# Kernel optimization log

Hardware: AMD Instinct MI355X
Metric: run time of the kernel (lower is better)

Reference implementation:

```python
import jax, jax.numpy as jnp
import numpy as np

N = 50000       # nodes
E = 800000      # edges
IN = 128        # in_channels
HID = 64        # hidden_channels
OUT = 32        # out_channels
H = 4           # heads
EH = 64         # edge_hidden_channels
EOUT = 2        # edge_out_channels
NEG_SLOPE = 0.2 # PyG GATConv default


def gat_conv(x, edge_index, W, att_src, att_dst, bias, num_nodes):
    """PyG GATConv, concat=False, add_self_loops=False, eval mode (no dropout).
    edge_attr is ignored because edge_dim=None (lin_edge is None in PyG).
    Returns (out [N, C], alpha [E, H])."""
    heads, C = att_src.shape
    xl = (x @ W).reshape(-1, heads, C)                 # [N, H, C]
    src, dst = edge_index[0], edge_index[1]
    a_src = jnp.sum(xl * att_src, axis=-1)             # [N, H]
    a_dst = jnp.sum(xl * att_dst, axis=-1)             # [N, H]
    alpha = jax.nn.leaky_relu(a_src[src] + a_dst[dst], NEG_SLOPE)  # [E, H]
    # segment softmax over destination nodes
    amax = jax.ops.segment_max(alpha, dst, num_segments=num_nodes)
    amax = jnp.where(jnp.isfinite(amax), amax, 0.0)
    ex = jnp.exp(alpha - amax[dst])
    denom = jax.ops.segment_sum(ex, dst, num_segments=num_nodes)
    alpha_n = ex / (denom[dst] + 1e-16)                # [E, H]
    msg = xl[src] * alpha_n[:, :, None]                # [E, H, C]
    out = jax.ops.segment_sum(msg, dst, num_segments=num_nodes)  # [N, H, C]
    out = out.mean(axis=1) + bias                      # concat=False -> head mean
    return out, alpha_n


def setup_inputs() -> dict:
    key = jax.random.key(0)
    ks = jax.random.split(key, 16)
    x = jax.random.normal(ks[0], (N, IN), dtype=jnp.float32)
    edge_index = jax.random.randint(ks[1], (2, E), 0, N, dtype=jnp.int32)
    edge_attr = jax.random.normal(ks[2], (E, 5), dtype=jnp.float32)
    s = lambda fan: 1.0 / np.sqrt(fan)
    W1 = jax.random.normal(ks[3], (IN, H * HID), dtype=jnp.float32) * s(IN)
    att1_src = jax.random.normal(ks[4], (H, HID), dtype=jnp.float32) * s(HID)
    att1_dst = jax.random.normal(ks[5], (H, HID), dtype=jnp.float32) * s(HID)
    b1 = jnp.zeros((HID,), dtype=jnp.float32)
    W3 = jax.random.normal(ks[6], (HID, H * OUT), dtype=jnp.float32) * s(HID)
    att3_src = jax.random.normal(ks[7], (H, OUT), dtype=jnp.float32) * s(OUT)
    att3_dst = jax.random.normal(ks[8], (H, OUT), dtype=jnp.float32) * s(OUT)
    b3 = jnp.zeros((OUT,), dtype=jnp.float32)
    EIN = 2 * OUT + H  # cat(out_src, alpha, out_dst)
    mW1 = jax.random.normal(ks[9], (EIN, EH), dtype=jnp.float32) * s(EIN)
    mb1 = jnp.zeros((EH,), dtype=jnp.float32)
    mW2 = jax.random.normal(ks[10], (EH, EOUT), dtype=jnp.float32) * s(EH)
    mb2 = jnp.zeros((EOUT,), dtype=jnp.float32)
    return {"x": x, "edge_index": edge_index, "edge_attr": edge_attr,
            "return_attention_weights": 1,
            "W1": W1, "att1_src": att1_src, "att1_dst": att1_dst, "b1": b1,
            "W3": W3, "att3_src": att3_src, "att3_dst": att3_dst, "b3": b3,
            "mW1": mW1, "mb1": mb1, "mW2": mW2, "mb2": mb2}


def reference(x, edge_index, edge_attr, return_attention_weights,
              W1, att1_src, att1_dst, b1, W3, att3_src, att3_dst, b3,
              mW1, mb1, mW2, mb2):
    edge_len = edge_attr.shape[0]  # == E (no self loops added)
    out, alpha = gat_conv(x, edge_index, W1, att1_src, att1_dst, b1, N)
    out, alpha = gat_conv(out, edge_index, W3, att3_src, att3_dst, b3, N)
    # F.dropout with training=False is the identity (eval mode)
    ei = edge_index[:, :edge_len]
    al = alpha[:edge_len, :]
    out_src = out[ei[0]]                                # [E, OUT]
    out_dst = out[ei[1]]                                # [E, OUT]
    edge_feat = jnp.concatenate([out_src, al, out_dst], axis=-1)  # [E, 2*OUT+H]
    h = jax.nn.relu(edge_feat @ mW1 + mb1)
    edge_out = h @ mW2 + mb2                            # [E, EOUT]
    return (out, edge_out)
```

## Files before the change

### kernel.cpp

```cpp
#include <hip/hip_runtime.h>
#include <hip/hip_fp16.h>

constexpr int NN   = 50000;
constexpr int EE   = 800000;
constexpr int INF  = 128;
constexpr int NH   = 4;
constexpr int GR64 = (NN + 63) / 64;
constexpr int EB   = (EE + 255) / 256;
constexpr int NCH  = (NN + 255) / 256;

struct __align__(8) h4 { __half2 a, b; };

__device__ __forceinline__ float elw(float a) {
    a = (a > 0.f) ? a : 0.2f * a;
    return __expf(a);
}


template <int CH, bool HOUT>
__device__ __forceinline__ void gemm_att_tile48(const float* __restrict__ A,
                                                const float* __restrict__ B,
                                                void* __restrict__ Cv,
                                                const float* __restrict__ att_s,
                                                const float* __restrict__ att_d,
                                                float* __restrict__ a_s,
                                                float* __restrict__ a_d,
                                                int N, int K, int M,
                                                int row0, int col0, int tid,
                                                float (*As)[68], float (*Bs)[132]) {
    const int tx = tid & 15, ty = tid >> 4;
    float acc[4][8] = {};

    for (int k0 = 0; k0 < K; k0 += 16) {
        {
            const int a_row = tid >> 2;
            const int a_k   = (tid & 3) * 4;
            const int gr    = row0 + a_row;
            float4 v = make_float4(0.f, 0.f, 0.f, 0.f);
            if (gr < N) v = *(const float4*)(A + (size_t)gr * K + k0 + a_k);
            As[a_k + 0][a_row] = v.x;
            As[a_k + 1][a_row] = v.y;
            As[a_k + 2][a_row] = v.z;
            As[a_k + 3][a_row] = v.w;
        }
        {
            const int b_k = tid >> 4;
            const int b_c = (tid & 15) * 8;
            const float* bp = B + (size_t)(k0 + b_k) * M + col0 + b_c;
            *(float4*)&Bs[b_k][b_c]     = *(const float4*)bp;
            *(float4*)&Bs[b_k][b_c + 4] = *(const float4*)(bp + 4);
        }
        __syncthreads();
        #pragma unroll
        for (int kk = 0; kk < 16; ++kk) {
            const float4 a  = *(const float4*)&As[kk][ty * 4];
            const float4 b0 = *(const float4*)&Bs[kk][tx * 4];
            const float4 b1 = *(const float4*)&Bs[kk][64 + tx * 4];
            const float av[4] = {a.x, a.y, a.z, a.w};
            const float bv[8] = {b0.x,b0.y,b0.z,b0.w,b1.x,b1.y,b1.z,b1.w};
            #pragma unroll
            for (int i = 0; i < 4; ++i)
                #pragma unroll
                for (int j = 0; j < 8; ++j)
                    acc[i][j] = fmaf(av[i], bv[j], acc[i][j]);
        }
        __syncthreads();
    }

    const int c0 = col0 + tx * 4;
    const int c1 = c0 + 64;
    const int head0 = c0 / CH, pos0 = c0 % CH;
    const int head1 = c1 / CH, pos1 = c1 % CH;
    float attS[8], attD[8];
    #pragma unroll
    for (int j = 0; j < 4; ++j) {
        attS[j]     = att_s[head0 * CH + pos0 + j];
        attD[j]     = att_d[head0 * CH + pos0 + j];
        attS[j + 4] = att_s[head1 * CH + pos1 + j];
        attD[j + 4] = att_d[head1 * CH + pos1 + j];
    }
    #pragma unroll
    for (int i = 0; i < 4; ++i) {
        const int r = row0 + ty * 4 + i;
        if (r < N) {
            if constexpr (HOUT) {
                __half* C = (__half*)Cv;
                __half* cp0 = C + (size_t)r * M + c0;
                __half* cp1 = C + (size_t)r * M + c1;
                *(__half2*)(cp0)     = __halves2half2(__float2half_rn(acc[i][0]), __float2half_rn(acc[i][1]));
                *(__half2*)(cp0 + 2) = __halves2half2(__float2half_rn(acc[i][2]), __float2half_rn(acc[i][3]));
                *(__half2*)(cp1)     = __halves2half2(__float2half_rn(acc[i][4]), __float2half_rn(acc[i][5]));
                *(__half2*)(cp1 + 2) = __halves2half2(__float2half_rn(acc[i][6]), __float2half_rn(acc[i][7]));
            } else {
                float* C = (float*)Cv;
                *(float4*)(C + (size_t)r * M + c0) = make_float4(acc[i][0], acc[i][1], acc[i][2], acc[i][3]);
                *(float4*)(C + (size_t)r * M + c1) = make_float4(acc[i][4], acc[i][5], acc[i][6], acc[i][7]);
            }
        }
        float ss0 = 0.f, sd0 = 0.f, ss1 = 0.f, sd1 = 0.f;
        #pragma unroll
        for (int j = 0; j < 4; ++j) {
            ss0 = fmaf(acc[i][j], attS[j], ss0);
            sd0 = fmaf(acc[i][j], attD[j], sd0);
            ss1 = fmaf(acc[i][j + 4], attS[j + 4], ss1);
            sd1 = fmaf(acc[i][j + 4], attD[j + 4], sd1);
        }
        #pragma unroll
        for (int msk = 1; msk < CH / 4; msk <<= 1) {
            ss0 += __shfl_xor(ss0, msk, 64);
            sd0 += __shfl_xor(sd0, msk, 64);
            ss1 += __shfl_xor(ss1, msk, 64);
            sd1 += __shfl_xor(sd1, msk, 64);
        }
        if ((tx & (CH / 4 - 1)) == 0 && r < N) {
            a_s[r * NH + head0] = ss0;
            a_d[r * NH + head0] = sd0;
            a_s[r * NH + head1] = ss1;
            a_d[r * NH + head1] = sd1;
        }
    }
}

__device__ __forceinline__ void gemm_pq_tile48(const float* __restrict__ A,
                                               const float* __restrict__ B,
                                               __half* __restrict__ C,
                                               int N, int K, int M,
                                               int row0, int col0, int tid,
                                               float (*As)[68], float (*Bs)[132]) {
    const int tx = tid & 15, ty = tid >> 4;
    float acc[4][8] = {};
    for (int k0 = 0; k0 < K; k0 += 16) {
        {
            const int a_row = tid >> 2;
            const int a_k   = (tid & 3) * 4;
            const int gr    = row0 + a_row;
            float4 v = make_float4(0.f, 0.f, 0.f, 0.f);
            if (gr < N) v = *(const float4*)(A + (size_t)gr * K + k0 + a_k);
            As[a_k + 0][a_row] = v.x;
            As[a_k + 1][a_row] = v.y;
            As[a_k + 2][a_row] = v.z;
            As[a_k + 3][a_row] = v.w;
        }
        {
            const int b_k = tid >> 4;
            const int b_c = (tid & 15) * 8;
            const float* bp = B + (size_t)(k0 + b_k) * M + col0 + b_c;
            *(float4*)&Bs[b_k][b_c]     = *(const float4*)bp;
            *(float4*)&Bs[b_k][b_c + 4] = *(const float4*)(bp + 4);
        }
        __syncthreads();
        #pragma unroll
        for (int kk = 0; kk < 16; ++kk) {
            const float4 a  = *(const float4*)&As[kk][ty * 4];
            const float4 b0 = *(const float4*)&Bs[kk][tx * 4];
            const float4 b1 = *(const float4*)&Bs[kk][64 + tx * 4];
            const float av[4] = {a.x, a.y, a.z, a.w};
            const float bv[8] = {b0.x,b0.y,b0.z,b0.w,b1.x,b1.y,b1.z,b1.w};
            #pragma unroll
            for (int i = 0; i < 4; ++i)
                #pragma unroll
                for (int j = 0; j < 8; ++j)
                    acc[i][j] = fmaf(av[i], bv[j], acc[i][j]);
        }
        __syncthreads();
    }
    const int c0 = col0 + tx * 4;
    const int c1 = c0 + 64;
    #pragma unroll
    for (int i = 0; i < 4; ++i) {
        const int r = row0 + ty * 4 + i;
        if (r < N) {
            __half* cp0 = C + (size_t)r * M + c0;
            __half* cp1 = C + (size_t)r * M + c1;
            *(__half2*)(cp0)     = __halves2half2(__float2half_rn(acc[i][0]), __float2half_rn(acc[i][1]));
            *(__half2*)(cp0 + 2) = __halves2half2(__float2half_rn(acc[i][2]), __float2half_rn(acc[i][3]));
            *(__half2*)(cp1)     = __halves2half2(__float2half_rn(acc[i][4]), __float2half_rn(acc[i][5]));
            *(__half2*)(cp1 + 2) = __halves2half2(__float2half_rn(acc[i][6]), __float2half_rn(acc[i][7]));
        }
    }
}


__device__ __forceinline__ void softagg1_node(int n, int lane,
                                              const int* __restrict__ rowptr,
                                              const int* __restrict__ psrc,
                                              const float* __restrict__ a_s,
                                              const float* __restrict__ a_d,
                                              const __half* __restrict__ xl,
                                              const float* __restrict__ bias,
                                              float* __restrict__ out) {
    const int r0 = rowptr[n], r1 = rowptr[n + 1];
    const int hh = lane >> 4;
    const float ad = a_d[n * NH + hh];

    const h4* X = (const h4*)xl;
    float4 A0 = {0,0,0,0}, A1 = {0,0,0,0}, A2 = {0,0,0,0}, A3 = {0,0,0,0};
    float sum = 0.f;
    int j = r0;
    for (; j + 7 < r1; j += 8) {
        const int s0 = psrc[j],     s1 = psrc[j + 1], s2 = psrc[j + 2], s3 = psrc[j + 3];
        const int s4 = psrc[j + 4], s5 = psrc[j + 5], s6 = psrc[j + 6], s7 = psrc[j + 7];
        const float w0 = elw(a_s[s0 * NH + hh] + ad);
        const float w1 = elw(a_s[s1 * NH + hh] + ad);
        const float w2 = elw(a_s[s2 * NH + hh] + ad);
        const float w3 = elw(a_s[s3 * NH + hh] + ad);
        const float w4 = elw(a_s[s4 * NH + hh] + ad);
        const float w5 = elw(a_s[s5 * NH + hh] + ad);
        const float w6 = elw(a_s[s6 * NH + hh] + ad);
        const float w7 = elw(a_s[s7 * NH + hh] + ad);
        sum += ((w0 + w1) + (w2 + w3)) + ((w4 + w5) + (w6 + w7));
        const h4 v0 = X[(size_t)s0 * 64 + lane];
        const h4 v1 = X[(size_t)s1 * 64 + lane];
        const h4 v2 = X[(size_t)s2 * 64 + lane];
        const h4 v3 = X[(size_t)s3 * 64 + lane];
        const h4 v4 = X[(size_t)s4 * 64 + lane];
        const h4 v5 = X[(size_t)s5 * 64 + lane];
        const h4 v6 = X[(size_t)s6 * 64 + lane];
        const h4 v7 = X[(size_t)s7 * 64 + lane];
        float2 l0 = __half22float2(v0.a), m0 = __half22float2(v0.b);
        float2 l1 = __half22float2(v1.a), m1 = __half22float2(v1.b);
        float2 l2 = __half22float2(v2.a), m2 = __half22float2(v2.b);
        float2 l3 = __half22float2(v3.a), m3 = __half22float2(v3.b);
        float2 l4 = __half22float2(v4.a), m4 = __half22float2(v4.b);
        float2 l5 = __half22float2(v5.a), m5 = __half22float2(v5.b);
        float2 l6 = __half22float2(v6.a), m6 = __half22float2(v6.b);
        float2 l7 = __half22float2(v7.a), m7 = __half22float2(v7.b);
        A0.x = fmaf(w0, l0.x, A0.x); A0.y = fmaf(w0, l0.y, A0.y);
        A0.z = fmaf(w0, m0.x, A0.z); A0.w = fmaf(w0, m0.y, A0.w);
        A1.x = fmaf(w1, l1.x, A1.x); A1.y = fmaf(w1, l1.y, A1.y);
        A1.z = fmaf(w1, m1.x, A1.z); A1.w = fmaf(w1, m1.y, A1.w);
        A2.x = fmaf(w2, l2.x, A2.x); A2.y = fmaf(w2, l2.y, A2.y);
        A2.z = fmaf(w2, m2.x, A2.z); A2.w = fmaf(w2, m2.y, A2.w);
        A3.x = fmaf(w3, l3.x, A3.x); A3.y = fmaf(w3, l3.y, A3.y);
        A3.z = fmaf(w3, m3.x, A3.z); A3.w = fmaf(w3, m3.y, A3.w);
        A0.x = fmaf(w4, l4.x, A0.x); A0.y = fmaf(w4, l4.y, A0.y);
        A0.z = fmaf(w4, m4.x, A0.z); A0.w = fmaf(w4, m4.y, A0.w);
        A1.x = fmaf(w5, l5.x, A1.x); A1.y = fmaf(w5, l5.y, A1.y);
        A1.z = fmaf(w5, m5.x, A1.z); A1.w = fmaf(w5, m5.y, A1.w);
        A2.x = fmaf(w6, l6.x, A2.x); A2.y = fmaf(w6, l6.y, A2.y);
        A2.z = fmaf(w6, m6.x, A2.z); A2.w = fmaf(w6, m6.y, A2.w);
        A3.x = fmaf(w7, l7.x, A3.x); A3.y = fmaf(w7, l7.y, A3.y);
        A3.z = fmaf(w7, m7.x, A3.z); A3.w = fmaf(w7, m7.y, A3.w);
    }
    for (; j < r1; ++j) {
        const int s0 = psrc[j];
        const float w0 = elw(a_s[s0 * NH + hh] + ad);
        sum += w0;
        const h4 v0 = X[(size_t)s0 * 64 + lane];
        float2 l0 = __half22float2(v0.a), m0 = __half22float2(v0.b);
        A0.x = fmaf(w0, l0.x, A0.x); A0.y = fmaf(w0, l0.y, A0.y);
        A0.z = fmaf(w0, m0.x, A0.z); A0.w = fmaf(w0, m0.y, A0.w);
    }
    const float inv = 1.f / (sum + 1e-30f);
    float4 t;
    t.x = ((A0.x + A1.x) + (A2.x + A3.x)) * inv;
    t.y = ((A0.y + A1.y) + (A2.y + A3.y)) * inv;
    t.z = ((A0.z + A1.z) + (A2.z + A3.z)) * inv;
    t.w = ((A0.w + A1.w) + (A2.w + A3.w)) * inv;
    #pragma unroll
    for (int msk = 16; msk < 64; msk <<= 1) {
        t.x += __shfl_xor(t.x, msk, 64);
        t.y += __shfl_xor(t.y, msk, 64);
        t.z += __shfl_xor(t.z, msk, 64);
        t.w += __shfl_xor(t.w, msk, 64);
    }
    if (lane < 16) {
        const float4 b = ((const float4*)bias)[lane];
        float4 o;
        o.x = t.x * 0.25f + b.x; o.y = t.y * 0.25f + b.y;
        o.z = t.z * 0.25f + b.z; o.w = t.w * 0.25f + b.w;
        ((float4*)out)[(size_t)n * 16 + lane] = o;
    }
}

__device__ __forceinline__ void softagg2_node(int n, int lane,
                                              const int* __restrict__ rowptr,
                                              const int* __restrict__ psrc,
                                              const float* __restrict__ a_s,
                                              const float* __restrict__ a_d,
                                              float* __restrict__ alpha_p,
                                              float* __restrict__ inv_s,
                                              const __half* __restrict__ xl,
                                              const float* __restrict__ bias,
                                              float* __restrict__ out) {
    const int r0 = rowptr[n], r1 = rowptr[n + 1];
    const int cl = lane & 31, half = lane >> 5, hh = cl >> 3;
    const float ad = a_d[n * NH + hh];
    const bool writer = (cl & 7) == 0;

    const h4* X = (const h4*)xl;
    float4 A0 = {0,0,0,0}, A1 = {0,0,0,0};
    float sum = 0.f;
    int j = r0;
    for (; j + 7 < r1; j += 8) {
        const int ja = j + half, jc = j + 2 + half, je = j + 4 + half, jg = j + 6 + half;
        const int sa = psrc[ja], sc = psrc[jc], se = psrc[je], sg = psrc[jg];
        const float wa = elw(a_s[sa * NH + hh] + ad);
        const float wc = elw(a_s[sc * NH + hh] + ad);
        const float we = elw(a_s[se * NH + hh] + ad);
        const float wg = elw(a_s[sg * NH + hh] + ad);
        if (writer) {
            alpha_p[ja * NH + hh] = wa; alpha_p[jc * NH + hh] = wc;
            alpha_p[je * NH + hh] = we; alpha_p[jg * NH + hh] = wg;
        }
        sum += (wa + wc) + (we + wg);
        const h4 va = X[(size_t)sa * 32 + cl];
        const h4 vc = X[(size_t)sc * 32 + cl];
        const h4 ve = X[(size_t)se * 32 + cl];
        const h4 vg = X[(size_t)sg * 32 + cl];
        const float2 la = __half22float2(va.a), ma = __half22float2(va.b);
        const float2 lc = __half22float2(vc.a), mc = __half22float2(vc.b);
        const float2 le = __half22float2(ve.a), me = __half22float2(ve.b);
        const float2 lg = __half22float2(vg.a), mg = __half22float2(vg.b);
        A0.x = fmaf(wa, la.x, A0.x); A0.y = fmaf(wa, la.y, A0.y);
        A0.z = fmaf(wa, ma.x, A0.z); A0.w = fmaf(wa, ma.y, A0.w);
        A1.x = fmaf(wc, lc.x, A1.x); A1.y = fmaf(wc, lc.y, A1.y);
        A1.z = fmaf(wc, mc.x, A1.z); A1.w = fmaf(wc, mc.y, A1.w);
        A0.x = fmaf(we, le.x, A0.x); A0.y = fmaf(we, le.y, A0.y);
        A0.z = fmaf(we, me.x, A0.z); A0.w = fmaf(we, me.y, A0.w);
        A1.x = fmaf(wg, lg.x, A1.x); A1.y = fmaf(wg, lg.y, A1.y);
        A1.z = fmaf(wg, mg.x, A1.z); A1.w = fmaf(wg, mg.y, A1.w);
    }
    for (; j < r1; j += 2) {
        const int ja = j + half;
        const bool valid = ja < r1;
        const int sa = psrc[valid ? ja : r0];
        float wa = 0.f;
        if (valid) {
            wa = elw(a_s[sa * NH + hh] + ad);
            if (writer) alpha_p[ja * NH + hh] = wa;
        }
        sum += wa;
        const h4 va = X[(size_t)sa * 32 + cl];
        const float2 la = __half22float2(va.a), ma = __half22float2(va.b);
        A0.x = fmaf(wa, la.x, A0.x); A0.y = fmaf(wa, la.y, A0.y);
        A0.z = fmaf(wa, ma.x, A0.z); A0.w = fmaf(wa, ma.y, A0.w);
    }
    sum += __shfl_xor(sum, 32, 64);
    const float inv = 1.f / (sum + 1e-30f);
    if (writer && half == 0) inv_s[n * NH + hh] = inv;

    float4 t;
    t.x = A0.x + A1.x; t.y = A0.y + A1.y; t.z = A0.z + A1.z; t.w = A0.w + A1.w;
    t.x += __shfl_xor(t.x, 32, 64);
    t.y += __shfl_xor(t.y, 32, 64);
    t.z += __shfl_xor(t.z, 32, 64);
    t.w += __shfl_xor(t.w, 32, 64);
    t.x *= inv; t.y *= inv; t.z *= inv; t.w *= inv;
    #pragma unroll
    for (int q = 0; q < 2; ++q) {
        const int msk = (q == 0) ? 8 : 16;
        t.x += __shfl_xor(t.x, msk, 64);
        t.y += __shfl_xor(t.y, msk, 64);
        t.z += __shfl_xor(t.z, msk, 64);
        t.w += __shfl_xor(t.w, msk, 64);
    }
    if (lane < 8) {
        const float4 b = ((const float4*)bias)[lane];
        float4 o;
        o.x = t.x * 0.25f + b.x; o.y = t.y * 0.25f + b.y;
        o.z = t.z * 0.25f + b.z; o.w = t.w * 0.25f + b.w;
        ((float4*)out)[(size_t)n * 8 + lane] = o;
    }
}


__global__ __launch_bounds__(256) void csr_gemm1_k(const int* __restrict__ ei,
                                                   int* __restrict__ deg,
                                                   const float* __restrict__ mW1,
                                                   float* __restrict__ W1pq,
                                                   const float* __restrict__ x,
                                                   const float* __restrict__ W1,
                                                   __half* __restrict__ xlh,
                                                   const float* __restrict__ att1s,
                                                   const float* __restrict__ att1d,
                                                   float* __restrict__ a_s,
                                                   float* __restrict__ a_d) {
    __shared__ float As[16][68];
    __shared__ float Bs[16][132];
    const int b = blockIdx.x;
    if (b < EB) {
        const int e = b * 256 + threadIdx.x;
        if (e < EE) atomicAdd(&deg[ei[EE + e]], 1);
    } else if (b < EB + 16) {
        const int idx = (b - EB) * 256 + threadIdx.x;
        if (idx < 32 * 128) {
            const int k = idx >> 7, jj = idx & 127;
            W1pq[idx] = (jj < 64) ? mW1[k * 64 + jj] : mW1[(36 + k) * 64 + (jj - 64)];
        }
    } else {
        const int t = b - EB - 16;
        gemm_att_tile48<64, true>(x, W1, xlh, att1s, att1d, a_s, a_d,
                                  NN, INF, NH * 64,
                                  (t % GR64) * 64, (t / GR64) * 128,
                                  threadIdx.x, As, Bs);
    }
}

template <int CH, bool HOUT>
__global__ __launch_bounds__(256) void gemm_att48_k(const float* __restrict__ A,
                                                    const float* __restrict__ B,
                                                    void* __restrict__ Cv,
                                                    const float* __restrict__ att_s,
                                                    const float* __restrict__ att_d,
                                                    float* __restrict__ a_s,
                                                    float* __restrict__ a_d,
                                                    int N, int K, int M) {
    __shared__ float As[16][68];
    __shared__ float Bs[16][132];
    gemm_att_tile48<CH, HOUT>(A, B, Cv, att_s, att_d, a_s, a_d, N, K, M,
                              blockIdx.x * 64, blockIdx.y * 128, threadIdx.x, As, Bs);
}

__global__ __launch_bounds__(256) void gemm_pq48_k(const float* __restrict__ A,
                                                   const float* __restrict__ B,
                                                   __half* __restrict__ C,
                                                   int N, int K, int M) {
    __shared__ float As[16][68];
    __shared__ float Bs[16][132];
    gemm_pq_tile48(A, B, C, N, K, M, blockIdx.x * 64, blockIdx.y * 128, threadIdx.x, As, Bs);
}

__global__ __launch_bounds__(256) void scan1_k(const int* __restrict__ deg,
                                               int* __restrict__ bsum) {
    __shared__ int sw[4];
    const int tid = threadIdx.x, lane = tid & 63, wv = tid >> 6;
    const int i = blockIdx.x * 256 + tid;
    int s = (i < NN) ? deg[i] : 0;
    #pragma unroll
    for (int d = 1; d < 64; d <<= 1) s += __shfl_xor(s, d, 64);
    if (lane == 0) sw[wv] = s;
    __syncthreads();
    if (tid == 0) bsum[blockIdx.x] = sw[0] + sw[1] + sw[2] + sw[3];
}

__global__ __launch_bounds__(256) void scan2_k(const int* __restrict__ bsum,
                                               int* __restrict__ boff) {
    __shared__ int sw[8];
    const int tid = threadIdx.x, lane = tid & 63, wv = tid >> 6;
    int v = (tid < NCH) ? bsum[tid] : 0;
    int incl = v;
    #pragma unroll
    for (int d = 1; d < 64; d <<= 1) {
        int t = __shfl_up(incl, d, 64);
        if (lane >= d) incl += t;
    }
    if (lane == 63) sw[wv] = incl;
    __syncthreads();
    if (wv == 0 && lane < 4) {
        int s4 = sw[lane];
        #pragma unroll
        for (int d = 1; d < 4; d <<= 1) {
            int t = __shfl_up(s4, d, 64);
            if (lane >= d) s4 += t;
        }
        sw[lane + 4] = s4;
    }
    __syncthreads();
    const int woff = (wv > 0) ? sw[wv - 1 + 4] : 0;
    if (tid < NCH) boff[tid] = woff + incl - v;
}

__global__ __launch_bounds__(256) void scan3_k(const int* __restrict__ deg,
                                               const int* __restrict__ boff,
                                               int* __restrict__ rowptr,
                                               int* __restrict__ cursor) {
    __shared__ int sw[8];
    const int tid = threadIdx.x, lane = tid & 63, wv = tid >> 6;
    const int c = blockIdx.x;
    const int i = c * 256 + tid;
    int v = (i < NN) ? deg[i] : 0;
    int incl = v;
    #pragma unroll
    for (int d = 1; d < 64; d <<= 1) {
        int t = __shfl_up(incl, d, 64);
        if (lane >= d) incl += t;
    }
    if (lane == 63) sw[wv] = incl;
    __syncthreads();
    if (wv == 0 && lane < 4) {
        int s4 = sw[lane];
        #pragma unroll
        for (int d = 1; d < 4; d <<= 1) {
            int t = __shfl_up(s4, d, 64);
            if (lane >= d) s4 += t;
        }
        sw[lane + 4] = s4;
    }
    __syncthreads();
    const int excl = boff[c] + ((wv > 0) ? sw[wv - 1 + 4] : 0) + incl - v;
    if (i < NN) { rowptr[i] = excl; cursor[i] = excl; }
    if (c == 0 && tid == 0) rowptr[NN] = EE;
}

__global__ __launch_bounds__(256) void scatter_perm_k(const int* __restrict__ ei,
                                                      int* __restrict__ cursor,
                                                      int* __restrict__ perm,
                                                      int* __restrict__ psrc,
                                                      int* __restrict__ pdst) {
    const int e = blockIdx.x * 256 + threadIdx.x;
    if (e >= EE) return;
    const int d = ei[EE + e];
    const int p = atomicAdd(&cursor[d], 1);
    perm[p] = e;
    psrc[p] = ei[e];
    pdst[p] = d;
}

__global__ __launch_bounds__(256) void softagg1h_k(const int* __restrict__ rowptr,
                                                   const int* __restrict__ psrc,
                                                   const float* __restrict__ a_s,
                                                   const float* __restrict__ a_d,
                                                   const __half* __restrict__ xl,
                                                   const float* __restrict__ bias,
                                                   float* __restrict__ out) {
    const int n = blockIdx.x * 4 + (threadIdx.x >> 6);
    if (n >= NN) return;
    softagg1_node(n, threadIdx.x & 63, rowptr, psrc, a_s, a_d, xl, bias, out);
}

__global__ __launch_bounds__(256) void softagg2h_k(const int* __restrict__ rowptr,
                                                   const int* __restrict__ psrc,
                                                   const float* __restrict__ a_s,
                                                   const float* __restrict__ a_d,
                                                   float* __restrict__ alpha_p,
                                                   float* __restrict__ inv_s,
                                                   const __half* __restrict__ xl,
                                                   const float* __restrict__ bias,
                                                   float* __restrict__ out) {
    const int n = blockIdx.x * 4 + (threadIdx.x >> 6);
    if (n >= NN) return;
    softagg2_node(n, threadIdx.x & 63, rowptr, psrc, a_s, a_d, alpha_p, inv_s, xl, bias, out);
}

__global__ __launch_bounds__(256) void edge_mlp_k(const __half* __restrict__ PQ,
                                                  const float* __restrict__ alpha_p,
                                                  const float* __restrict__ inv_s,
                                                  const int* __restrict__ psrc,
                                                  const int* __restrict__ pdst,
                                                  const int* __restrict__ perm,
                                                  const float* __restrict__ mW1,
                                                  const float* __restrict__ mb1,
                                                  const float* __restrict__ mW2,
                                                  const float* __restrict__ mb2,
                                                  float* __restrict__ out) {
    const int lane = threadIdx.x & 63, wvv = threadIdx.x >> 6;
    const int g = lane >> 4, c = lane & 15;

    const float4 wa0 = *(const float4*)&mW1[32 * 64 + c * 4];
    const float4 wa1 = *(const float4*)&mW1[33 * 64 + c * 4];
    const float4 wa2 = *(const float4*)&mW1[34 * 64 + c * 4];
    const float4 wa3 = *(const float4*)&mW1[35 * 64 + c * 4];
    const float4 b1v = *(const float4*)&mb1[c * 4];
    const float4 w2a = *(const float4*)&mW2[c * 8];
    const float4 w2b = *(const float4*)&mW2[c * 8 + 4];
    const float bo0 = mb2[0], bo1 = mb2[1];

    const h4* PQ4 = (const h4*)PQ;
    const int gw = blockIdx.x * 4 + wvv;
    const int stride4 = gridDim.x * 4 * 4;

    for (int jb = gw * 4; jb < EE; jb += stride4) {
        const int j = jb + g;
        const int s = psrc[j];
        const int d = pdst[j];
        const float4 ar = *(const float4*)&alpha_p[(size_t)j * 4];
        const float4 iv = *(const float4*)&inv_s[(size_t)d * 4];
        const float al0 = ar.x * iv.x, al1 = ar.y * iv.y;
        const float al2 = ar.z * iv.z, al3 = ar.w * iv.w;
        const h4 ph = PQ4[(size_t)s * 32 + c];
        const h4 qh = PQ4[(size_t)d * 32 + 16 + c];
        const float2 pl = __half22float2(ph.a), pm = __half22float2(ph.b);
        const float2 ql = __half22float2(qh.a), qm = __half22float2(qh.b);
        float4 h;
        h.x = pl.x + ql.x + b1v.x; h.y = pl.y + ql.y + b1v.y;
        h.z = pm.x + qm.x + b1v.z; h.w = pm.y + qm.y + b1v.w;
        h.x = fmaf(al0, wa0.x, h.x); h.y = fmaf(al0, wa0.y, h.y);
        h.z = fmaf(al0, wa0.z, h.z); h.w = fmaf(al0, wa0.w, h.w);
        h.x = fmaf(al1, wa1.x, h.x); h.y = fmaf(al1, wa1.y, h.y);
        h.z = fmaf(al1, wa1.z, h.z); h.w = fmaf(al1, wa1.w, h.w);
        h.x = fmaf(al2, wa2.x, h.x); h.y = fmaf(al2, wa2.y, h.y);
        h.z = fmaf(al2, wa2.z, h.z); h.w = fmaf(al2, wa2.w, h.w);
        h.x = fmaf(al3, wa3.x, h.x); h.y = fmaf(al3, wa3.y, h.y);
        h.z = fmaf(al3, wa3.z, h.z); h.w = fmaf(al3, wa3.w, h.w);
        h.x = fmaxf(h.x, 0.f); h.y = fmaxf(h.y, 0.f);
        h.z = fmaxf(h.z, 0.f); h.w = fmaxf(h.w, 0.f);

        float v0 = h.x * w2a.x + h.y * w2a.z + h.z * w2b.x + h.w * w2b.z;
        float v1 = h.x * w2a.y + h.y * w2a.w + h.z * w2b.y + h.w * w2b.w;
        #pragma unroll
        for (int msk = 1; msk < 16; msk <<= 1) {
            v0 += __shfl_xor(v0, msk, 64);
            v1 += __shfl_xor(v1, msk, 64);
        }
        if (c == 0)
            *(float2*)&out[(size_t)perm[j] * 2] = make_float2(v0 + bo0, v1 + bo1);
    }
}

extern "C" void kernel_launch(void* const* d_in, const int* in_sizes, int n_in,
                              void* d_out, int out_size, void* d_ws, size_t ws_size,
                              hipStream_t stream) {
    const float* x        = (const float*)d_in[0];
    const int*   ei       = (const int*)d_in[1];
    const float* W1       = (const float*)d_in[4];
    const float* att1_src = (const float*)d_in[5];
    const float* att1_dst = (const float*)d_in[6];
    const float* b1       = (const float*)d_in[7];
    const float* W3       = (const float*)d_in[8];
    const float* att3_src = (const float*)d_in[9];
    const float* att3_dst = (const float*)d_in[10];
    const float* b3       = (const float*)d_in[11];
    const float* mW1      = (const float*)d_in[12];
    const float* mb1      = (const float*)d_in[13];
    const float* mW2      = (const float*)d_in[14];
    const float* mb2      = (const float*)d_in[15];

    float* out_nodes = (float*)d_out;
    float* out_edges = out_nodes + (size_t)NN * 32;

    float* ws = (float*)d_ws;
    __half*   xlh     = (__half*)ws;
    __half*   xl2h    = (__half*)ws;
    __half*   PQh     = (__half*)ws;
    float*    h1      = ws + 12800000;
    float*    alpha_p = ws + 16000000;
    float*    a_s     = ws + 25600000;
    float*    a_d     = ws + 25800000;
    float*    W1pq    = ws + 26000000;
    float*    inv_s   = ws + 26100000;
    int*      bsum    = (int*)(ws + 26300000);
    int*      boff    = (int*)(ws + 26301000);
    int*      deg     = (int*)(ws + 26400000);
    int*      cursor  = (int*)(ws + 26450000);
    int*      rowptr  = (int*)(ws + 26500000);
    int*      perm    = (int*)(ws + 26550008);
    int*      psrc    = (int*)(ws + 27350008);
    int*      pdst    = (int*)(ws + 28150008);

    const int NB4 = (NN + 3) / 4;

    hipMemsetAsync(deg, 0, (size_t)NN * 4, stream);
    csr_gemm1_k<<<EB + 16 + GR64 * 2, 256, 0, stream>>>(ei, deg, mW1, W1pq,
                                                        x, W1, xlh,
                                                        att1_src, att1_dst, a_s, a_d);
    scan1_k<<<NCH, 256, 0, stream>>>(deg, bsum);
    scan2_k<<<1, 256, 0, stream>>>(bsum, boff);
    scan3_k<<<NCH, 256, 0, stream>>>(deg, boff, rowptr, cursor);
    scatter_perm_k<<<EB, 256, 0, stream>>>(ei, cursor, perm, psrc, pdst);
    softagg1h_k<<<NB4, 256, 0, stream>>>(rowptr, psrc, a_s, a_d, xlh, b1, h1);
    gemm_att48_k<32, true><<<dim3(GR64, 1), 256, 0, stream>>>(h1, W3, xl2h,
                                                              att3_src, att3_dst,
                                                              a_s, a_d, NN, 64, NH * 32);
    softagg2h_k<<<NB4, 256, 0, stream>>>(rowptr, psrc, a_s, a_d, alpha_p, inv_s, xl2h, b3,
                                         out_nodes);
    gemm_pq48_k<<<dim3(GR64, 1), 256, 0, stream>>>(out_nodes, W1pq, PQh, NN, 32, 128);
    edge_mlp_k<<<2048, 256, 0, stream>>>(PQh, alpha_p, inv_s, psrc, pdst, perm,
                                         mW1, mb1, mW2, mb2, out_edges);
}
```

Before: 447.6 us.

## Double GEMM K-tile depth to 32 and split fused degree/GEMM kernel

The shared-memory GEMM tiles now load a K-slice of 32 per iteration instead of 16, halving the number of barrier-separated load/compute steps and doubling LDS use per block. The combined kernel that did degree counting, weight packing and the first GEMM is split into three separate launches, with the GEMM now launched through the templated gemm_att48_k kernel. This removes branch divergence and lets the GEMM kernel allocate larger LDS without penalizing the atomic blocks, at the cost of extra launches and less overlap between the degree atomics and GEMM work.

New measurement: 450.0 us. Within noise of the previous version (+0.5%).

```diff
diff --git a/kernel.cpp b/kernel.cpp
--- a/kernel.cpp
+++ b/kernel.cpp
@@ -31,28 +31,35 @@
     const int tx = tid & 15, ty = tid >> 4;
     float acc[4][8] = {};
 
-    for (int k0 = 0; k0 < K; k0 += 16) {
+    for (int k0 = 0; k0 < K; k0 += 32) {
         {
             const int a_row = tid >> 2;
-            const int a_k   = (tid & 3) * 4;
+            const int a_k   = (tid & 3) * 8;
             const int gr    = row0 + a_row;
-            float4 v = make_float4(0.f, 0.f, 0.f, 0.f);
-            if (gr < N) v = *(const float4*)(A + (size_t)gr * K + k0 + a_k);
-            As[a_k + 0][a_row] = v.x;
-            As[a_k + 1][a_row] = v.y;
-            As[a_k + 2][a_row] = v.z;
-            As[a_k + 3][a_row] = v.w;
+            float4 v0 = make_float4(0.f,0.f,0.f,0.f), v1 = make_float4(0.f,0.f,0.f,0.f);
+            if (gr < N) {
+                const float* ap = A + (size_t)gr * K + k0 + a_k;
+                v0 = *(const float4*)ap;
+                v1 = *(const float4*)(ap + 4);
+            }
+            As[a_k + 0][a_row] = v0.x; As[a_k + 1][a_row] = v0.y;
+            As[a_k + 2][a_row] = v0.z; As[a_k + 3][a_row] = v0.w;
+            As[a_k + 4][a_row] = v1.x; As[a_k + 5][a_row] = v1.y;
+            As[a_k + 6][a_row] = v1.z; As[a_k + 7][a_row] = v1.w;
         }
         {
             const int b_k = tid >> 4;
             const int b_c = (tid & 15) * 8;
-            const float* bp = B + (size_t)(k0 + b_k) * M + col0 + b_c;
-            *(float4*)&Bs[b_k][b_c]     = *(const float4*)bp;
-            *(float4*)&Bs[b_k][b_c + 4] = *(const float4*)(bp + 4);
+            const float* bp0 = B + (size_t)(k0 + b_k) * M + col0 + b_c;
+            const float* bp1 = B + (size_t)(k0 + b_k + 16) * M + col0 + b_c;
+            *(float4*)&Bs[b_k][b_c]          = *(const float4*)bp0;
+            *(float4*)&Bs[b_k][b_c + 4]      = *(const float4*)(bp0 + 4);
+            *(float4*)&Bs[b_k + 16][b_c]     = *(const float4*)bp1;
+            *(float4*)&Bs[b_k + 16][b_c + 4] = *(const float4*)(bp1 + 4);
         }
         __syncthreads();
         #pragma unroll
-        for (int kk = 0; kk < 16; ++kk) {
+        for (int kk = 0; kk < 32; ++kk) {
             const float4 a  = *(const float4*)&As[kk][ty * 4];
             const float4 b0 = *(const float4*)&Bs[kk][tx * 4];
             const float4 b1 = *(const float4*)&Bs[kk][64 + tx * 4];
@@ -129,28 +136,35 @@
                                                float (*As)[68], float (*Bs)[132]) {
     const int tx = tid & 15, ty = tid >> 4;
     float acc[4][8] = {};
-    for (int k0 = 0; k0 < K; k0 += 16) {
+    for (int k0 = 0; k0 < K; k0 += 32) {
         {
             const int a_row = tid >> 2;
-            const int a_k   = (tid & 3) * 4;
+            const int a_k   = (tid & 3) * 8;
             const int gr    = row0 + a_row;
-            float4 v = make_float4(0.f, 0.f, 0.f, 0.f);
-            if (gr < N) v = *(const float4*)(A + (size_t)gr * K + k0 + a_k);
-            As[a_k + 0][a_row] = v.x;
-            As[a_k + 1][a_row] = v.y;
-            As[a_k + 2][a_row] = v.z;
-            As[a_k + 3][a_row] = v.w;
+            float4 v0 = make_float4(0.f,0.f,0.f,0.f), v1 = make_float4(0.f,0.f,0.f,0.f);
+            if (gr < N) {
+                const float* ap = A + (size_t)gr * K + k0 + a_k;
+                v0 = *(const float4*)ap;
+                v1 = *(const float4*)(ap + 4);
+            }
+            As[a_k + 0][a_row] = v0.x; As[a_k + 1][a_row] = v0.y;
+            As[a_k + 2][a_row] = v0.z; As[a_k + 3][a_row] = v0.w;
+            As[a_k + 4][a_row] = v1.x; As[a_k + 5][a_row] = v1.y;
+            As[a_k + 6][a_row] = v1.z; As[a_k + 7][a_row] = v1.w;
         }
         {
             const int b_k = tid >> 4;
             const int b_c = (tid & 15) * 8;
-            const float* bp = B + (size_t)(k0 + b_k) * M + col0 + b_c;
-            *(float4*)&Bs[b_k][b_c]     = *(const float4*)bp;
-            *(float4*)&Bs[b_k][b_c + 4] = *(const float4*)(bp + 4);
+            const float* bp0 = B + (size_t)(k0 + b_k) * M + col0 + b_c;
+            const float* bp1 = B + (size_t)(k0 + b_k + 16) * M + col0 + b_c;
+            *(float4*)&Bs[b_k][b_c]          = *(const float4*)bp0;
+            *(float4*)&Bs[b_k][b_c + 4]      = *(const float4*)(bp0 + 4);
+            *(float4*)&Bs[b_k + 16][b_c]     = *(const float4*)bp1;
+            *(float4*)&Bs[b_k + 16][b_c + 4] = *(const float4*)(bp1 + 4);
         }
         __syncthreads();
         #pragma unroll
-        for (int kk = 0; kk < 16; ++kk) {
+        for (int kk = 0; kk < 32; ++kk) {
             const float4 a  = *(const float4*)&As[kk][ty * 4];
             const float4 b0 = *(const float4*)&Bs[kk][tx * 4];
             const float4 b1 = *(const float4*)&Bs[kk][64 + tx * 4];
@@ -365,36 +379,18 @@
 }
 
 
-__global__ __launch_bounds__(256) void csr_gemm1_k(const int* __restrict__ ei,
-                                                   int* __restrict__ deg,
-                                                   const float* __restrict__ mW1,
-                                                   float* __restrict__ W1pq,
-                                                   const float* __restrict__ x,
-                                                   const float* __restrict__ W1,
-                                                   __half* __restrict__ xlh,
-                                                   const float* __restrict__ att1s,
-                                                   const float* __restrict__ att1d,
-                                                   float* __restrict__ a_s,
-                                                   float* __restrict__ a_d) {
-    __shared__ float As[16][68];
-    __shared__ float Bs[16][132];
-    const int b = blockIdx.x;
-    if (b < EB) {
-        const int e = b * 256 + threadIdx.x;
-        if (e < EE) atomicAdd(&deg[ei[EE + e]], 1);
-    } else if (b < EB + 16) {
-        const int idx = (b - EB) * 256 + threadIdx.x;
-        if (idx < 32 * 128) {
-            const int k = idx >> 7, jj = idx & 127;
-            W1pq[idx] = (jj < 64) ? mW1[k * 64 + jj] : mW1[(36 + k) * 64 + (jj - 64)];
-        }
-    } else {
-        const int t = b - EB - 16;
-        gemm_att_tile48<64, true>(x, W1, xlh, att1s, att1d, a_s, a_d,
-                                  NN, INF, NH * 64,
-                                  (t % GR64) * 64, (t / GR64) * 128,
-                                  threadIdx.x, As, Bs);
-    }
+__global__ __launch_bounds__(256) void count_deg_k(const int* __restrict__ ei,
+                                                   int* __restrict__ deg) {
+    const int e = blockIdx.x * 256 + threadIdx.x;
+    if (e < EE) atomicAdd(&deg[ei[EE + e]], 1);
+}
+
+__global__ __launch_bounds__(256) void pack_w1_k(const float* __restrict__ mW1,
+                                                 float* __restrict__ W1pq) {
+    const int idx = blockIdx.x * 256 + threadIdx.x;
+    if (idx >= 32 * 128) return;
+    const int k = idx >> 7, j = idx & 127;
+    W1pq[idx] = (j < 64) ? mW1[k * 64 + j] : mW1[(36 + k) * 64 + (j - 64)];
 }
 
 template <int CH, bool HOUT>
@@ -406,8 +402,8 @@
                                                     float* __restrict__ a_s,
                                                     float* __restrict__ a_d,
                                                     int N, int K, int M) {
-    __shared__ float As[16][68];
-    __shared__ float Bs[16][132];
+    __shared__ float As[32][68];
+    __shared__ float Bs[32][132];
     gemm_att_tile48<CH, HOUT>(A, B, Cv, att_s, att_d, a_s, a_d, N, K, M,
                               blockIdx.x * 64, blockIdx.y * 128, threadIdx.x, As, Bs);
 }
@@ -416,8 +412,8 @@
                                                    const float* __restrict__ B,
                                                    __half* __restrict__ C,
                                                    int N, int K, int M) {
-    __shared__ float As[16][68];
-    __shared__ float Bs[16][132];
+    __shared__ float As[32][68];
+    __shared__ float Bs[32][132];
     gemm_pq_tile48(A, B, C, N, K, M, blockIdx.x * 64, blockIdx.y * 128, threadIdx.x, As, Bs);
 }
 
@@ -641,9 +637,11 @@
     const int NB4 = (NN + 3) / 4;
 
     hipMemsetAsync(deg, 0, (size_t)NN * 4, stream);
-    csr_gemm1_k<<<EB + 16 + GR64 * 2, 256, 0, stream>>>(ei, deg, mW1, W1pq,
-                                                        x, W1, xlh,
-                                                        att1_src, att1_dst, a_s, a_d);
+    count_deg_k<<<EB, 256, 0, stream>>>(ei, deg);
+    pack_w1_k<<<16, 256, 0, stream>>>(mW1, W1pq);
+    gemm_att48_k<64, true><<<dim3(GR64, 2), 256, 0, stream>>>(x, W1, xlh,
+                                                              att1_src, att1_dst,
+                                                              a_s, a_d, NN, INF, NH * 64);
     scan1_k<<<NCH, 256, 0, stream>>>(deg, bsum);
     scan2_k<<<1, 256, 0, stream>>>(bsum, boff);
     scan3_k<<<NCH, 256, 0, stream>>>(deg, boff, rowptr, cursor);
```
